# Kernel tuning notes

Hardware: AMD Instinct MI355X
Metric: run time of the kernel (lower is better)

Reference implementation:

```python
import jax, jax.numpy as jnp
import numpy as np

N = 100000
F = 128

def shifted_softplus(x):
    return jax.nn.softplus(x) - jnp.log(2.0).astype(x.dtype)

def setup_inputs() -> dict:
    key = jax.random.key(0)
    ks = jax.random.split(key, 8)
    scale = 1.0 / np.sqrt(F)
    s = jax.random.normal(ks[0], (N, F), dtype=jnp.float32)
    v = jax.random.normal(ks[1], (N, F, 3), dtype=jnp.float32)
    U_w = jax.random.uniform(ks[2], (F, F), dtype=jnp.float32, minval=-scale, maxval=scale)
    V_w = jax.random.uniform(ks[3], (F, F), dtype=jnp.float32, minval=-scale, maxval=scale)
    scale2 = 1.0 / np.sqrt(2 * F)
    a_w1 = jax.random.uniform(ks[4], (F, 2 * F), dtype=jnp.float32, minval=-scale2, maxval=scale2)
    a_b1 = jax.random.uniform(ks[5], (F,), dtype=jnp.float32, minval=-scale2, maxval=scale2)
    a_w2 = jax.random.uniform(ks[6], (3 * F, F), dtype=jnp.float32, minval=-scale, maxval=scale)
    a_b2 = jax.random.uniform(ks[7], (3 * F,), dtype=jnp.float32, minval=-scale, maxval=scale)
    return {"s": s, "v": v, "U_w": U_w, "V_w": V_w,
            "a_w1": a_w1, "a_b1": a_b1, "a_w2": a_w2, "a_b2": a_b2}

def reference(s, v, U_w, V_w, a_w1, a_b1, a_w2, a_b2):
    # Vector linears along feature dim: (N,F,3) x (Fout,Fin) -> (N,F,3)
    Uv = jnp.einsum('nfc,gf->ngc', v, U_w)
    Vv = jnp.einsum('nfc,gf->ngc', v, V_w)
    Vv_norm_sq = jnp.sum(Vv * Vv, axis=-1)          # (N,F)
    mlp_in = jnp.concatenate([s, Vv_norm_sq], axis=-1)  # (N,2F)
    h = shifted_softplus(mlp_in @ a_w1.T + a_b1)     # (N,F)
    a = h @ a_w2.T + a_b2                            # (N,3F)
    a_ss, a_sv, a_vv = jnp.split(a, 3, axis=-1)
    inner = jnp.sum(Uv * Vv, axis=-1)                # (N,F)
    s_new = s + a_ss + a_sv * inner
    v_new = v + a_vv[:, :, None] * Uv
    return (s_new, v_new)
```

## Files before the change

kernel.cpp:

```cpp
#include <hip/hip_runtime.h>

#define F 128
#define TILE 32
#define NTHR 512
#define NBLK 256

typedef __attribute__((ext_vector_type(8))) __bf16 bf16x8;
typedef __attribute__((ext_vector_type(4))) float f32x4;
typedef __attribute__((ext_vector_type(8))) unsigned short us8;
typedef __attribute__((ext_vector_type(4))) unsigned short us4;
typedef __attribute__((ext_vector_type(2))) unsigned short us2;

struct f3 { float x, y, z; };

__device__ __forceinline__ unsigned short f2bf(float x) {
    __bf16 h = (__bf16)x;
    return __builtin_bit_cast(unsigned short, h);
}
__device__ __forceinline__ float bf2f(unsigned short u) {
    unsigned x = ((unsigned)u) << 16;
    return __builtin_bit_cast(float, x);
}
__device__ __forceinline__ bf16x8 pack8(float4 a, float4 b) {
    us8 t;
    t[0] = f2bf(a.x); t[1] = f2bf(a.y); t[2] = f2bf(a.z); t[3] = f2bf(a.w);
    t[4] = f2bf(b.x); t[5] = f2bf(b.y); t[6] = f2bf(b.z); t[7] = f2bf(b.w);
    return __builtin_bit_cast(bf16x8, t);
}

__device__ __forceinline__ void gload16(const float* g, const unsigned short* l) {
    __builtin_amdgcn_global_load_lds(
        (const __attribute__((address_space(1))) void*)g,
        (__attribute__((address_space(3))) void*)l, 16, 0, 0);
}

#define RAWV 0
#define A1B  24576
#define A1S  136
#define A2B  37632
#define A2S  264
#define A3B  46080
#define A3S  136
#define SHSZ 50432

__global__ __launch_bounds__(256)
void prep_w(const float* __restrict__ Uw, const float* __restrict__ Vw,
            const float* __restrict__ aw1, const float* __restrict__ aw2,
            unsigned short* __restrict__ wbf)
{
    int i = (blockIdx.x * 256 + threadIdx.x) * 4;
    const float* src; int off;
    if (i < 16384)      { src = Uw;  off = i; }
    else if (i < 32768) { src = Vw;  off = i - 16384; }
    else if (i < 65536) { src = aw1; off = i - 32768; }
    else                { src = aw2; off = i - 65536; }
    float4 x = *(const float4*)&src[off];
    us4 o;
    o[0] = f2bf(x.x); o[1] = f2bf(x.y); o[2] = f2bf(x.z); o[3] = f2bf(x.w);
    *(us4*)&wbf[i] = o;
}

template<bool PRE>
__global__ __launch_bounds__(NTHR) __attribute__((amdgpu_waves_per_eu(2, 2)))
void painn_main(const float* __restrict__ s, const float* __restrict__ v,
                const float* __restrict__ Uw, const float* __restrict__ Vw,
                const float* __restrict__ aw1, const float* __restrict__ ab1,
                const float* __restrict__ aw2, const float* __restrict__ ab2,
                const unsigned short* __restrict__ wbf,
                float* __restrict__ out, int Ntot)
{
    __shared__ __align__(16) unsigned short SH[SHSZ];

    const int tid  = threadIdx.x;
    const int lane = tid & 63;
    const int w    = tid >> 6;
    const int l15  = lane & 15;
    const int kp   = lane >> 4;
    const int col  = (w << 4) | l15;
    const size_t NF = (size_t)Ntot * F;
    const int NT   = Ntot / TILE;

    const unsigned short* wU  = wbf;
    const unsigned short* wV  = wbf + 16384;
    const unsigned short* wW1 = wbf + 32768;
    const unsigned short* wW2 = wbf + 65536;

    const float b1  = ab1[col];
    const float bss = ab2[col];
    const float bsv = ab2[F + col];
    const float bvv = ab2[2 * F + col];

    const int vf0  = lane << 1;
    const int srow = tid >> 4;
    const int sf0  = (tid & 15) << 3;

    const float* rawv = (const float*)&SH[RAWV];

    float4 sp0, sp1;

    {
        int t0 = blockIdx.x;
        const float* vsrc = v + (size_t)t0 * TILE * 384;
        #pragma unroll
        for (int j = 0; j < 6; ++j) {
            int ofs = (w + j * 8) * 256;
            gload16(vsrc + ofs + lane * 4, &SH[RAWV + ofs * 2]);
        }
        const float* ssrc = s + (size_t)t0 * TILE * 128 + srow * 128 + sf0;
        sp0 = *(const float4*)ssrc;
        sp1 = *(const float4*)(ssrc + 4);
    }
    asm volatile("s_waitcnt vmcnt(0)" ::: "memory");

    for (int t = blockIdx.x; t < NT; t += NBLK) {
        asm volatile("s_waitcnt vmcnt(8)" ::: "memory");
        __builtin_amdgcn_s_barrier();

        bf16x8 bU[4], bV[4], bW1[8], bWs[4], bWt[4], bWv[4];
        if constexpr (PRE) {
            #pragma unroll
            for (int ks = 0; ks < 4; ++ks) {
                int k0 = (ks << 5) + (kp << 3);
                bU[ks]  = *(const bf16x8*)&wU[col * F + k0];
                bV[ks]  = *(const bf16x8*)&wV[col * F + k0];
                bWs[ks] = *(const bf16x8*)&wW2[(0 * F + col) * F + k0];
                bWt[ks] = *(const bf16x8*)&wW2[(1 * F + col) * F + k0];
                bWv[ks] = *(const bf16x8*)&wW2[(2 * F + col) * F + k0];
            }
            #pragma unroll
            for (int ks = 0; ks < 8; ++ks) {
                int k0 = (ks << 5) + (kp << 3);
                bW1[ks] = *(const bf16x8*)&wW1[col * 256 + k0];
            }
        } else {
            #pragma unroll
            for (int ks = 0; ks < 4; ++ks) {
                int k0 = (ks << 5) + (kp << 3);
                const float4* p;
                p = (const float4*)&Uw[col * F + k0];              bU[ks]  = pack8(p[0], p[1]);
                p = (const float4*)&Vw[col * F + k0];              bV[ks]  = pack8(p[0], p[1]);
                p = (const float4*)&aw2[(size_t)(0*F+col)*F + k0]; bWs[ks] = pack8(p[0], p[1]);
                p = (const float4*)&aw2[(size_t)(1*F+col)*F + k0]; bWt[ks] = pack8(p[0], p[1]);
                p = (const float4*)&aw2[(size_t)(2*F+col)*F + k0]; bWv[ks] = pack8(p[0], p[1]);
            }
            #pragma unroll
            for (int ks = 0; ks < 8; ++ks) {
                int k0 = (ks << 5) + (kp << 3);
                const float4* p = (const float4*)&aw1[col * 256 + k0];
                bW1[ks] = pack8(p[0], p[1]);
            }
        }
        __builtin_amdgcn_sched_barrier(0);

        #pragma unroll
        for (int it = 0; it < 4; ++it) {
            int nl = w + (it << 3);
            const float2* src = (const float2*)&rawv[nl * 384 + vf0 * 3];
            float2 ab = src[0], cd = src[1], ef = src[2];
            us2 p;
            p[0] = f2bf(ab.x); p[1] = f2bf(cd.y); *(us2*)&SH[A1B + (0 * TILE + nl) * A1S + vf0] = p;
            p[0] = f2bf(ab.y); p[1] = f2bf(ef.x); *(us2*)&SH[A1B + (1 * TILE + nl) * A1S + vf0] = p;
            p[0] = f2bf(cd.x); p[1] = f2bf(ef.y); *(us2*)&SH[A1B + (2 * TILE + nl) * A1S + vf0] = p;
        }
        {
            us4 t0, t1;
            t0[0] = f2bf(sp0.x); t0[1] = f2bf(sp0.y); t0[2] = f2bf(sp0.z); t0[3] = f2bf(sp0.w);
            t1[0] = f2bf(sp1.x); t1[1] = f2bf(sp1.y); t1[2] = f2bf(sp1.z); t1[3] = f2bf(sp1.w);
            *(us4*)&SH[A2B + srow * A2S + sf0]     = t0;
            *(us4*)&SH[A2B + srow * A2S + sf0 + 4] = t1;
        }
        asm volatile("s_waitcnt lgkmcnt(0)" ::: "memory");
        __builtin_amdgcn_s_barrier();
        __builtin_amdgcn_sched_barrier(0);

        if (t + NBLK < NT) {
            int t2 = t + NBLK;
            const float* vsrc = v + (size_t)t2 * TILE * 384;
            #pragma unroll
            for (int j = 0; j < 6; ++j) {
                int ofs = (w + j * 8) * 256;
                gload16(vsrc + ofs + lane * 4, &SH[RAWV + ofs * 2]);
            }
            const float* ssrc = s + (size_t)t2 * TILE * 128 + srow * 128 + sf0;
            sp0 = *(const float4*)ssrc;
            sp1 = *(const float4*)(ssrc + 4);
        }
        __builtin_amdgcn_sched_barrier(0);

        float inr[2][4], nrm[2][4];
        us4 pU[6];
        #pragma unroll
        for (int nt = 0; nt < 2; ++nt)
            #pragma unroll
            for (int r = 0; r < 4; ++r) { inr[nt][r] = 0.f; nrm[nt][r] = 0.f; }
        #pragma unroll
        for (int c = 0; c < 3; ++c) {
            f32x4 aU[2], aV[2];
            aU[0] = (f32x4){0.f,0.f,0.f,0.f}; aU[1] = (f32x4){0.f,0.f,0.f,0.f};
            aV[0] = (f32x4){0.f,0.f,0.f,0.f}; aV[1] = (f32x4){0.f,0.f,0.f,0.f};
            #pragma unroll
            for (int ks = 0; ks < 4; ++ks) {
                #pragma unroll
                for (int nt = 0; nt < 2; ++nt) {
                    bf16x8 a = *(const bf16x8*)&SH[A1B + ((c * 2 + nt) * 16 + l15) * A1S + (ks << 5) + (kp << 3)];
                    aU[nt] = __builtin_amdgcn_mfma_f32_16x16x32_bf16(a, bU[ks], aU[nt], 0, 0, 0);
                    aV[nt] = __builtin_amdgcn_mfma_f32_16x16x32_bf16(a, bV[ks], aV[nt], 0, 0, 0);
                }
            }
            #pragma unroll
            for (int nt = 0; nt < 2; ++nt) {
                us4 q;
                #pragma unroll
                for (int r = 0; r < 4; ++r) {
                    nrm[nt][r] += aV[nt][r] * aV[nt][r];
                    inr[nt][r] += aU[nt][r] * aV[nt][r];
                    q[r] = f2bf(aU[nt][r]);
                }
                pU[c * 2 + nt] = q;
            }
        }
        #pragma unroll
        for (int nt = 0; nt < 2; ++nt) {
            #pragma unroll
            for (int r = 0; r < 4; ++r) {
                int row = nt * 16 + (kp << 2) + r;
                SH[A2B + row * A2S + 128 + col] = f2bf(nrm[nt][r]);
            }
        }
        asm volatile("s_waitcnt lgkmcnt(0)" ::: "memory");
        __builtin_amdgcn_s_barrier();

        f32x4 accH[2];
        accH[0] = (f32x4){0.f,0.f,0.f,0.f}; accH[1] = (f32x4){0.f,0.f,0.f,0.f};
        #pragma unroll
        for (int ks = 0; ks < 8; ++ks) {
            int k0 = (ks << 5) + (kp << 3);
            #pragma unroll
            for (int nt = 0; nt < 2; ++nt) {
                bf16x8 a = *(const bf16x8*)&SH[A2B + (nt * 16 + l15) * A2S + k0];
                accH[nt] = __builtin_amdgcn_mfma_f32_16x16x32_bf16(a, bW1[ks], accH[nt], 0, 0, 0);
            }
        }
        #pragma unroll
        for (int nt = 0; nt < 2; ++nt) {
            #pragma unroll
            for (int r = 0; r < 4; ++r) {
                float x = accH[nt][r] + b1;
                float hsp = fmaxf(x, 0.f) + __logf(1.f + __expf(-fabsf(x))) - 0.69314718056f;
                int row = nt * 16 + (kp << 2) + r;
                SH[A3B + row * A3S + col] = f2bf(hsp);
            }
        }
        asm volatile("s_waitcnt lgkmcnt(0)" ::: "memory");
        __builtin_amdgcn_s_barrier();

        f32x4 accA[2], accS[2], accT[2];
        #pragma unroll
        for (int i = 0; i < 2; ++i) {
            accA[i] = (f32x4){0.f,0.f,0.f,0.f};
            accS[i] = (f32x4){0.f,0.f,0.f,0.f};
            accT[i] = (f32x4){0.f,0.f,0.f,0.f};
        }
        #pragma unroll
        for (int ks = 0; ks < 4; ++ks) {
            int k0 = (ks << 5) + (kp << 3);
            #pragma unroll
            for (int nt = 0; nt < 2; ++nt) {
                bf16x8 a = *(const bf16x8*)&SH[A3B + (nt * 16 + l15) * A3S + k0];
                accS[nt] = __builtin_amdgcn_mfma_f32_16x16x32_bf16(a, bWs[ks], accS[nt], 0, 0, 0);
                accT[nt] = __builtin_amdgcn_mfma_f32_16x16x32_bf16(a, bWt[ks], accT[nt], 0, 0, 0);
                accA[nt] = __builtin_amdgcn_mfma_f32_16x16x32_bf16(a, bWv[ks], accA[nt], 0, 0, 0);
            }
        }

        #pragma unroll
        for (int nt = 0; nt < 2; ++nt) {
            #pragma unroll
            for (int r = 0; r < 4; ++r) {
                int nl = nt * 16 + (kp << 2) + r;
                int n  = t * TILE + nl;
                float avv = accA[nt][r] + bvv;
                size_t base = ((size_t)n * F + col) * 3;
                f3 val;
                val.x = bf2f(SH[A1B + (0 * TILE + nl) * A1S + col]) + avv * bf2f(pU[0 * 2 + nt][r]);
                val.y = bf2f(SH[A1B + (1 * TILE + nl) * A1S + col]) + avv * bf2f(pU[1 * 2 + nt][r]);
                val.z = bf2f(SH[A1B + (2 * TILE + nl) * A1S + col]) + avv * bf2f(pU[2 * 2 + nt][r]);
                *(f3*)&out[NF + base] = val;
                float sres = bf2f(SH[A2B + nl * A2S + col]);
                out[(size_t)n * F + col] = sres + (accS[nt][r] + bss) + (accT[nt][r] + bsv) * inr[nt][r];
            }
        }
    }
}

extern "C" void kernel_launch(void* const* d_in, const int* in_sizes, int n_in,
                              void* d_out, int out_size, void* d_ws, size_t ws_size,
                              hipStream_t stream) {
    (void)n_in; (void)out_size;
    const float* s   = (const float*)d_in[0];
    const float* v   = (const float*)d_in[1];
    const float* Uw  = (const float*)d_in[2];
    const float* Vw  = (const float*)d_in[3];
    const float* aw1 = (const float*)d_in[4];
    const float* ab1 = (const float*)d_in[5];
    const float* aw2 = (const float*)d_in[6];
    const float* ab2 = (const float*)d_in[7];
    float* out = (float*)d_out;
    int Ntot = in_sizes[0] / F;

    if (ws_size >= 114688u * sizeof(unsigned short)) {
        unsigned short* wbf = (unsigned short*)d_ws;
        hipLaunchKernelGGL(prep_w, dim3(112), dim3(256), 0, stream, Uw, Vw, aw1, aw2, wbf);
        hipLaunchKernelGGL((painn_main<true>), dim3(NBLK), dim3(NTHR), 0, stream,
                           s, v, Uw, Vw, aw1, ab1, aw2, ab2, wbf, out, Ntot);
    } else {
        hipLaunchKernelGGL((painn_main<false>), dim3(NBLK), dim3(NTHR), 0, stream,
                           s, v, Uw, Vw, aw1, ab1, aw2, ab2, (const unsigned short*)nullptr, out, Ntot);
    }
}
```

Before: 187.2 us.

## Split fused persistent kernel into three per-tile kernels with bf16 workspace intermediates

Replaces the single persistent fused kernel with three non-persistent kernels: one computes Vv norms and the U·V inner product, one runs the MLP and writes s_new, and one recomputes Uv and writes v_new. Each launches one block per tile and uses far less shared memory, allowing higher occupancy in place of the software-pipelined persistent loop. The cost is reading v twice, recomputing U·v, and round-tripping three N×F bf16 intermediates through global memory, plus extra launches and a larger workspace requirement. The fused kernel is kept as a fallback when the workspace is too small.

```diff
diff --git a/kernel.cpp b/kernel.cpp
--- a/kernel.cpp
+++ b/kernel.cpp
@@ -3,21 +3,23 @@
 #define F 128
 #define TILE 32
 #define NTHR 512
-#define NBLK 256
 
 typedef __attribute__((ext_vector_type(8))) __bf16 bf16x8;
 typedef __attribute__((ext_vector_type(4))) float f32x4;
 typedef __attribute__((ext_vector_type(8))) unsigned short us8;
 typedef __attribute__((ext_vector_type(4))) unsigned short us4;
 typedef __attribute__((ext_vector_type(2))) unsigned short us2;
+typedef unsigned short us;
 
 struct f3 { float x, y, z; };
 
-__device__ __forceinline__ unsigned short f2bf(float x) {
+#define MFMA(a,b,c) __builtin_amdgcn_mfma_f32_16x16x32_bf16((a),(b),(c),0,0,0)
+
+__device__ __forceinline__ us f2bf(float x) {
     __bf16 h = (__bf16)x;
-    return __builtin_bit_cast(unsigned short, h);
-}
-__device__ __forceinline__ float bf2f(unsigned short u) {
+    return __builtin_bit_cast(us, h);
+}
+__device__ __forceinline__ float bf2f(us u) {
     unsigned x = ((unsigned)u) << 16;
     return __builtin_bit_cast(float, x);
 }
@@ -27,26 +29,20 @@
     t[4] = f2bf(b.x); t[5] = f2bf(b.y); t[6] = f2bf(b.z); t[7] = f2bf(b.w);
     return __builtin_bit_cast(bf16x8, t);
 }
-
-__device__ __forceinline__ void gload16(const float* g, const unsigned short* l) {
+__device__ __forceinline__ void gload16(const float* g, const us* l) {
     __builtin_amdgcn_global_load_lds(
         (const __attribute__((address_space(1))) void*)g,
         (__attribute__((address_space(3))) void*)l, 16, 0, 0);
 }
-
-#define RAWV 0
-#define A1B  24576
-#define A1S  136
-#define A2B  37632
-#define A2S  264
-#define A3B  46080
-#define A3S  136
-#define SHSZ 50432
+__device__ __forceinline__ void bar_lgkm() {
+    asm volatile("s_waitcnt lgkmcnt(0)" ::: "memory");
+    __builtin_amdgcn_s_barrier();
+}
 
 __global__ __launch_bounds__(256)
 void prep_w(const float* __restrict__ Uw, const float* __restrict__ Vw,
             const float* __restrict__ aw1, const float* __restrict__ aw2,
-            unsigned short* __restrict__ wbf)
+            us* __restrict__ wbf)
 {
     int i = (blockIdx.x * 256 + threadIdx.x) * 4;
     const float* src; int off;
@@ -60,151 +56,377 @@
     *(us4*)&wbf[i] = o;
 }
 
+#define K_RAWV 0
+#define K_VRB  24576
+#define K_OUT  24576
+#define K_SHSZ 36864
+
+__device__ __forceinline__ int k_vr(int crow, int k) {
+    return K_VRB + (((crow << 7) + k) ^ ((crow & 7) << 3));
+}
+
+#define STAGE_AND_CONVERT(vptr, t)                                              \
+    {                                                                           \
+        const float* vsrc = (vptr) + (size_t)(t) * (TILE * 384);                \
+        _Pragma("unroll")                                                       \
+        for (int j = 0; j < 6; ++j) {                                           \
+            int ofs = (w + j * 8) * 256;                                        \
+            gload16(vsrc + ofs + lane * 4, &SH[K_RAWV + ofs * 2]);              \
+        }                                                                       \
+    }                                                                           \
+    asm volatile("s_waitcnt vmcnt(0)" ::: "memory");                            \
+    __builtin_amdgcn_s_barrier();                                               \
+    {                                                                           \
+        const float* rawv = (const float*)&SH[K_RAWV];                          \
+        _Pragma("unroll")                                                       \
+        for (int it = 0; it < 4; ++it) {                                        \
+            int idx = tid + it * 512, nl = idx >> 6, f0 = (idx & 63) << 1;      \
+            const float2* src = (const float2*)&rawv[nl * 384 + f0 * 3];        \
+            float2 ab = src[0], cd = src[1], ef = src[2];                       \
+            us2 p;                                                              \
+            p[0]=f2bf(ab.x); p[1]=f2bf(cd.y); *(us2*)&SH[k_vr(0*TILE+nl,f0)]=p; \
+            p[0]=f2bf(ab.y); p[1]=f2bf(ef.x); *(us2*)&SH[k_vr(1*TILE+nl,f0)]=p; \
+            p[0]=f2bf(cd.x); p[1]=f2bf(ef.y); *(us2*)&SH[k_vr(2*TILE+nl,f0)]=p; \
+        }                                                                       \
+    }                                                                           \
+    bar_lgkm();
+
+__global__ __launch_bounds__(NTHR, 4)
+void k1_uv(const float* __restrict__ v, const us* __restrict__ wbf,
+           us* __restrict__ wnrm, us* __restrict__ winr, int Ntot)
+{
+    __shared__ __align__(16) us SH[K_SHSZ];
+    const int tid = threadIdx.x, lane = tid & 63, w = tid >> 6;
+    const int l15 = lane & 15, kp = lane >> 4;
+    const int col = (w << 4) | l15;
+    const int t   = blockIdx.x;
+
+    STAGE_AND_CONVERT(v, t)
+
+    bf16x8 bU[4], bV[4];
+    #pragma unroll
+    for (int ks = 0; ks < 4; ++ks) {
+        int k0 = (ks << 5) + (kp << 3);
+        bU[ks] = *(const bf16x8*)&wbf[col * F + k0];
+        bV[ks] = *(const bf16x8*)&wbf[16384 + col * F + k0];
+    }
+    float nrm[2][4], inr[2][4];
+    #pragma unroll
+    for (int c = 0; c < 3; ++c) {
+        f32x4 aU[2], aV[2];
+        aU[0]=(f32x4){0,0,0,0}; aU[1]=(f32x4){0,0,0,0};
+        aV[0]=(f32x4){0,0,0,0}; aV[1]=(f32x4){0,0,0,0};
+        #pragma unroll
+        for (int ks = 0; ks < 4; ++ks) {
+            #pragma unroll
+            for (int nt = 0; nt < 2; ++nt) {
+                bf16x8 a = *(const bf16x8*)&SH[k_vr(c*TILE + nt*16 + l15, (ks<<5)+(kp<<3))];
+                aU[nt] = MFMA(a, bU[ks], aU[nt]);
+                aV[nt] = MFMA(a, bV[ks], aV[nt]);
+            }
+        }
+        #pragma unroll
+        for (int nt = 0; nt < 2; ++nt)
+            #pragma unroll
+            for (int r = 0; r < 4; ++r) {
+                float uu = aU[nt][r], vv = aV[nt][r];
+                if (c == 0) { nrm[nt][r] = vv*vv; inr[nt][r] = uu*vv; }
+                else        { nrm[nt][r] += vv*vv; inr[nt][r] += uu*vv; }
+            }
+    }
+    bar_lgkm();
+    #pragma unroll
+    for (int nt = 0; nt < 2; ++nt)
+        #pragma unroll
+        for (int r = 0; r < 4; ++r) {
+            int row = nt * 16 + (kp << 2) + r;
+            SH[K_OUT + row * 128 + col]        = f2bf(nrm[nt][r]);
+            SH[K_OUT + 4096 + row * 128 + col] = f2bf(inr[nt][r]);
+        }
+    bar_lgkm();
+    *(us8*)&wnrm[(size_t)t * 4096 + tid * 8] = *(const us8*)&SH[K_OUT + tid * 8];
+    *(us8*)&winr[(size_t)t * 4096 + tid * 8] = *(const us8*)&SH[K_OUT + 4096 + tid * 8];
+}
+
+#define M_A2S 264
+#define M_A3B 8448
+#define M_A3S 136
+#define M_SHSZ 12800
+
+__global__ __launch_bounds__(NTHR, 4)
+void k2_mlp(const float* __restrict__ s, const us* __restrict__ wbf,
+            const float* __restrict__ ab1, const float* __restrict__ ab2,
+            const us* __restrict__ wnrm, const us* __restrict__ winr,
+            us* __restrict__ wavv, float* __restrict__ out, int Ntot)
+{
+    __shared__ __align__(16) us SH[M_SHSZ];
+    const int tid = threadIdx.x, lane = tid & 63, w = tid >> 6;
+    const int l15 = lane & 15, kp = lane >> 4;
+    const int col = (w << 4) | l15;
+    const int t   = blockIdx.x;
+    const int srow = tid >> 4, sf0 = (tid & 15) << 3;
+
+    {
+        const float4* sp = (const float4*)&s[(size_t)t * TILE * 128 + srow * 128 + sf0];
+        float4 x = sp[0], y = sp[1];
+        us4 t0, t1;
+        t0[0]=f2bf(x.x); t0[1]=f2bf(x.y); t0[2]=f2bf(x.z); t0[3]=f2bf(x.w);
+        t1[0]=f2bf(y.x); t1[1]=f2bf(y.y); t1[2]=f2bf(y.z); t1[3]=f2bf(y.w);
+        *(us4*)&SH[srow * M_A2S + sf0]     = t0;
+        *(us4*)&SH[srow * M_A2S + sf0 + 4] = t1;
+        us8 nv = *(const us8*)&wnrm[(size_t)t * 4096 + tid * 8];
+        *(us8*)&SH[srow * M_A2S + 128 + sf0] = nv;
+    }
+    bar_lgkm();
+
+    f32x4 accH[2];
+    accH[0]=(f32x4){0,0,0,0}; accH[1]=(f32x4){0,0,0,0};
+    #pragma unroll
+    for (int ks = 0; ks < 8; ++ks) {
+        int k0 = (ks << 5) + (kp << 3);
+        bf16x8 bw = *(const bf16x8*)&wbf[32768 + col * 256 + k0];
+        #pragma unroll
+        for (int nt = 0; nt < 2; ++nt) {
+            bf16x8 a = *(const bf16x8*)&SH[(nt * 16 + l15) * M_A2S + k0];
+            accH[nt] = MFMA(a, bw, accH[nt]);
+        }
+    }
+    float b1 = ab1[col];
+    #pragma unroll
+    for (int nt = 0; nt < 2; ++nt)
+        #pragma unroll
+        for (int r = 0; r < 4; ++r) {
+            float x = accH[nt][r] + b1;
+            float hsp = fmaxf(x, 0.f) + __logf(1.f + __expf(-fabsf(x))) - 0.69314718056f;
+            int row = nt * 16 + (kp << 2) + r;
+            SH[M_A3B + row * M_A3S + col] = f2bf(hsp);
+        }
+    bar_lgkm();
+
+    f32x4 accS[2], accT[2], accA[2];
+    #pragma unroll
+    for (int i = 0; i < 2; ++i) {
+        accS[i]=(f32x4){0,0,0,0}; accT[i]=(f32x4){0,0,0,0}; accA[i]=(f32x4){0,0,0,0};
+    }
+    #pragma unroll
+    for (int ks = 0; ks < 4; ++ks) {
+        int k0 = (ks << 5) + (kp << 3);
+        bf16x8 bws = *(const bf16x8*)&wbf[65536 + (0 * F + col) * F + k0];
+        bf16x8 bwt = *(const bf16x8*)&wbf[65536 + (1 * F + col) * F + k0];
+        bf16x8 bwv = *(const bf16x8*)&wbf[65536 + (2 * F + col) * F + k0];
+        #pragma unroll
+        for (int nt = 0; nt < 2; ++nt) {
+            bf16x8 a = *(const bf16x8*)&SH[M_A3B + (nt * 16 + l15) * M_A3S + k0];
+            accS[nt] = MFMA(a, bws, accS[nt]);
+            accT[nt] = MFMA(a, bwt, accT[nt]);
+            accA[nt] = MFMA(a, bwv, accA[nt]);
+        }
+    }
+
+    float bss = ab2[col], bsv = ab2[F + col], bvv = ab2[2 * F + col];
+    #pragma unroll
+    for (int nt = 0; nt < 2; ++nt)
+        #pragma unroll
+        for (int r = 0; r < 4; ++r) {
+            int nl = nt * 16 + (kp << 2) + r;
+            size_t n = (size_t)t * TILE + nl;
+            float inner = bf2f(winr[n * 128 + col]);
+            float sres  = bf2f(SH[nl * M_A2S + col]);
+            out[n * 128 + col] = sres + (accS[nt][r] + bss) + (accT[nt][r] + bsv) * inner;
+        }
+    bar_lgkm();
+    #pragma unroll
+    for (int nt = 0; nt < 2; ++nt)
+        #pragma unroll
+        for (int r = 0; r < 4; ++r) {
+            int row = nt * 16 + (kp << 2) + r;
+            SH[row * 128 + col] = f2bf(accA[nt][r] + bvv);
+        }
+    bar_lgkm();
+    *(us8*)&wavv[(size_t)t * 4096 + tid * 8] = *(const us8*)&SH[tid * 8];
+}
+
+__global__ __launch_bounds__(NTHR, 4)
+void k3_vnew(const float* __restrict__ v, const us* __restrict__ wbf,
+             const us* __restrict__ wavv, float* __restrict__ out, int Ntot)
+{
+    __shared__ __align__(16) us SH[K_SHSZ];
+    const int tid = threadIdx.x, lane = tid & 63, w = tid >> 6;
+    const int l15 = lane & 15, kp = lane >> 4;
+    const int col = (w << 4) | l15;
+    const int t   = blockIdx.x;
+    const size_t NF = (size_t)Ntot * F;
+
+    STAGE_AND_CONVERT(v, t)
+
+    bf16x8 bU[4];
+    #pragma unroll
+    for (int ks = 0; ks < 4; ++ks) {
+        int k0 = (ks << 5) + (kp << 3);
+        bU[ks] = *(const bf16x8*)&wbf[col * F + k0];
+    }
+    us4 pU[3][2];
+    #pragma unroll
+    for (int c = 0; c < 3; ++c) {
+        f32x4 aU[2];
+        aU[0]=(f32x4){0,0,0,0}; aU[1]=(f32x4){0,0,0,0};
+        #pragma unroll
+        for (int ks = 0; ks < 4; ++ks) {
+            #pragma unroll
+            for (int nt = 0; nt < 2; ++nt) {
+                bf16x8 a = *(const bf16x8*)&SH[k_vr(c*TILE + nt*16 + l15, (ks<<5)+(kp<<3))];
+                aU[nt] = MFMA(a, bU[ks], aU[nt]);
+            }
+        }
+        #pragma unroll
+        for (int nt = 0; nt < 2; ++nt) {
+            us4 q;
+            #pragma unroll
+            for (int r = 0; r < 4; ++r) q[r] = f2bf(aU[nt][r]);
+            pU[c][nt] = q;
+        }
+    }
+
+    const float* rawv = (const float*)&SH[K_RAWV];
+    #pragma unroll
+    for (int nt = 0; nt < 2; ++nt)
+        #pragma unroll
+        for (int r = 0; r < 4; ++r) {
+            int nl = nt * 16 + (kp << 2) + r;
+            size_t n = (size_t)t * TILE + nl;
+            float avv = bf2f(wavv[n * 128 + col]);
+            f3 val;
+            val.x = rawv[nl * 384 + col * 3 + 0] + avv * bf2f(pU[0][nt][r]);
+            val.y = rawv[nl * 384 + col * 3 + 1] + avv * bf2f(pU[1][nt][r]);
+            val.z = rawv[nl * 384 + col * 3 + 2] + avv * bf2f(pU[2][nt][r]);
+            *(f3*)&out[NF + (n * 128 + col) * 3] = val;
+        }
+}
+
+#define FD_RAWV 0
+#define FD_A1B  24576
+#define FD_A1S  136
+#define FD_A2B  37632
+#define FD_A2S  264
+#define FD_A3B  46080
+#define FD_A3S  136
+#define FD_SHSZ 50432
+#define FD_NBLK 256
+
 template<bool PRE>
 __global__ __launch_bounds__(NTHR) __attribute__((amdgpu_waves_per_eu(2, 2)))
-void painn_main(const float* __restrict__ s, const float* __restrict__ v,
-                const float* __restrict__ Uw, const float* __restrict__ Vw,
-                const float* __restrict__ aw1, const float* __restrict__ ab1,
-                const float* __restrict__ aw2, const float* __restrict__ ab2,
-                const unsigned short* __restrict__ wbf,
-                float* __restrict__ out, int Ntot)
+void fused_fb(const float* __restrict__ s, const float* __restrict__ v,
+              const float* __restrict__ Uw, const float* __restrict__ Vw,
+              const float* __restrict__ aw1, const float* __restrict__ ab1,
+              const float* __restrict__ aw2, const float* __restrict__ ab2,
+              const us* __restrict__ wbf, float* __restrict__ out, int Ntot)
 {
-    __shared__ __align__(16) unsigned short SH[SHSZ];
-
-    const int tid  = threadIdx.x;
-    const int lane = tid & 63;
-    const int w    = tid >> 6;
-    const int l15  = lane & 15;
-    const int kp   = lane >> 4;
-    const int col  = (w << 4) | l15;
+    __shared__ __align__(16) us SH[FD_SHSZ];
+    const int tid = threadIdx.x, lane = tid & 63, w = tid >> 6;
+    const int l15 = lane & 15, kp = lane >> 4;
+    const int col = (w << 4) | l15;
     const size_t NF = (size_t)Ntot * F;
-    const int NT   = Ntot / TILE;
-
-    const unsigned short* wU  = wbf;
-    const unsigned short* wV  = wbf + 16384;
-    const unsigned short* wW1 = wbf + 32768;
-    const unsigned short* wW2 = wbf + 65536;
-
-    const float b1  = ab1[col];
-    const float bss = ab2[col];
-    const float bsv = ab2[F + col];
-    const float bvv = ab2[2 * F + col];
-
-    const int vf0  = lane << 1;
-    const int srow = tid >> 4;
-    const int sf0  = (tid & 15) << 3;
-
-    const float* rawv = (const float*)&SH[RAWV];
-
+    const int NT = Ntot / TILE;
+    const us* wU  = wbf;
+    const us* wV  = wbf + 16384;
+    const us* wW1 = wbf + 32768;
+    const us* wW2 = wbf + 65536;
+    const float b1 = ab1[col], bss = ab2[col], bsv = ab2[F+col], bvv = ab2[2*F+col];
+    const int srow = tid >> 4, sf0 = (tid & 15) << 3;
+    const float* rawv = (const float*)&SH[FD_RAWV];
     float4 sp0, sp1;
-
     {
         int t0 = blockIdx.x;
         const float* vsrc = v + (size_t)t0 * TILE * 384;
         #pragma unroll
         for (int j = 0; j < 6; ++j) {
             int ofs = (w + j * 8) * 256;
-            gload16(vsrc + ofs + lane * 4, &SH[RAWV + ofs * 2]);
+            gload16(vsrc + ofs + lane * 4, &SH[FD_RAWV + ofs * 2]);
         }
         const float* ssrc = s + (size_t)t0 * TILE * 128 + srow * 128 + sf0;
-        sp0 = *(const float4*)ssrc;
-        sp1 = *(const float4*)(ssrc + 4);
+        sp0 = *(const float4*)ssrc; sp1 = *(const float4*)(ssrc + 4);
     }
     asm volatile("s_waitcnt vmcnt(0)" ::: "memory");
-
-    for (int t = blockIdx.x; t < NT; t += NBLK) {
+    for (int t = blockIdx.x; t < NT; t += FD_NBLK) {
         asm volatile("s_waitcnt vmcnt(8)" ::: "memory");
         __builtin_amdgcn_s_barrier();
-
         bf16x8 bU[4], bV[4], bW1[8], bWs[4], bWt[4], bWv[4];
         if constexpr (PRE) {
             #pragma unroll
             for (int ks = 0; ks < 4; ++ks) {
                 int k0 = (ks << 5) + (kp << 3);
-                bU[ks]  = *(const bf16x8*)&wU[col * F + k0];
-                bV[ks]  = *(const bf16x8*)&wV[col * F + k0];
-                bWs[ks] = *(const bf16x8*)&wW2[(0 * F + col) * F + k0];
-                bWt[ks] = *(const bf16x8*)&wW2[(1 * F + col) * F + k0];
-                bWv[ks] = *(const bf16x8*)&wW2[(2 * F + col) * F + k0];
-            }
-            #pragma unroll
-            for (int ks = 0; ks < 8; ++ks) {
-                int k0 = (ks << 5) + (kp << 3);
-                bW1[ks] = *(const bf16x8*)&wW1[col * 256 + k0];
-            }
+                bU[ks] = *(const bf16x8*)&wU[col*F+k0];
+                bV[ks] = *(const bf16x8*)&wV[col*F+k0];
+                bWs[ks] = *(const bf16x8*)&wW2[(0*F+col)*F+k0];
+                bWt[ks] = *(const bf16x8*)&wW2[(1*F+col)*F+k0];
+                bWv[ks] = *(const bf16x8*)&wW2[(2*F+col)*F+k0];
+            }
+            #pragma unroll
+            for (int ks = 0; ks < 8; ++ks)
+                bW1[ks] = *(const bf16x8*)&wW1[col*256 + (ks<<5)+(kp<<3)];
         } else {
             #pragma unroll
             for (int ks = 0; ks < 4; ++ks) {
                 int k0 = (ks << 5) + (kp << 3);
                 const float4* p;
-                p = (const float4*)&Uw[col * F + k0];              bU[ks]  = pack8(p[0], p[1]);
-                p = (const float4*)&Vw[col * F + k0];              bV[ks]  = pack8(p[0], p[1]);
-                p = (const float4*)&aw2[(size_t)(0*F+col)*F + k0]; bWs[ks] = pack8(p[0], p[1]);
-                p = (const float4*)&aw2[(size_t)(1*F+col)*F + k0]; bWt[ks] = pack8(p[0], p[1]);
-                p = (const float4*)&aw2[(size_t)(2*F+col)*F + k0]; bWv[ks] = pack8(p[0], p[1]);
+                p = (const float4*)&Uw[col*F+k0];               bU[ks]=pack8(p[0],p[1]);
+                p = (const float4*)&Vw[col*F+k0];               bV[ks]=pack8(p[0],p[1]);
+                p = (const float4*)&aw2[(size_t)(0*F+col)*F+k0]; bWs[ks]=pack8(p[0],p[1]);
+                p = (const float4*)&aw2[(size_t)(1*F+col)*F+k0]; bWt[ks]=pack8(p[0],p[1]);
+                p = (const float4*)&aw2[(size_t)(2*F+col)*F+k0]; bWv[ks]=pack8(p[0],p[1]);
             }
             #pragma unroll
             for (int ks = 0; ks < 8; ++ks) {
-                int k0 = (ks << 5) + (kp << 3);
-                const float4* p = (const float4*)&aw1[col * 256 + k0];
+                const float4* p = (const float4*)&aw1[col*256 + (ks<<5)+(kp<<3)];
                 bW1[ks] = pack8(p[0], p[1]);
             }
         }
         __builtin_amdgcn_sched_barrier(0);
-
         #pragma unroll
         for (int it = 0; it < 4; ++it) {
             int nl = w + (it << 3);
-            const float2* src = (const float2*)&rawv[nl * 384 + vf0 * 3];
+            const float2* src = (const float2*)&rawv[nl * 384 + (lane << 1) * 3];
             float2 ab = src[0], cd = src[1], ef = src[2];
+            int vf0 = lane << 1;
             us2 p;
-            p[0] = f2bf(ab.x); p[1] = f2bf(cd.y); *(us2*)&SH[A1B + (0 * TILE + nl) * A1S + vf0] = p;
-            p[0] = f2bf(ab.y); p[1] = f2bf(ef.x); *(us2*)&SH[A1B + (1 * TILE + nl) * A1S + vf0] = p;
-            p[0] = f2bf(cd.x); p[1] = f2bf(ef.y); *(us2*)&SH[A1B + (2 * TILE + nl) * A1S + vf0] = p;
+            p[0]=f2bf(ab.x); p[1]=f2bf(cd.y); *(us2*)&SH[FD_A1B+(0*TILE+nl)*FD_A1S+vf0]=p;
+            p[0]=f2bf(ab.y); p[1]=f2bf(ef.x); *(us2*)&SH[FD_A1B+(1*TILE+nl)*FD_A1S+vf0]=p;
+            p[0]=f2bf(cd.x); p[1]=f2bf(ef.y); *(us2*)&SH[FD_A1B+(2*TILE+nl)*FD_A1S+vf0]=p;
         }
         {
             us4 t0, t1;
-            t0[0] = f2bf(sp0.x); t0[1] = f2bf(sp0.y); t0[2] = f2bf(sp0.z); t0[3] = f2bf(sp0.w);
-            t1[0] = f2bf(sp1.x); t1[1] = f2bf(sp1.y); t1[2] = f2bf(sp1.z); t1[3] = f2bf(sp1.w);
-            *(us4*)&SH[A2B + srow * A2S + sf0]     = t0;
-            *(us4*)&SH[A2B + srow * A2S + sf0 + 4] = t1;
-        }
-        asm volatile("s_waitcnt lgkmcnt(0)" ::: "memory");
-        __builtin_amdgcn_s_barrier();
-        __builtin_amdgcn_sched_barrier(0);
-
-        if (t + NBLK < NT) {
-            int t2 = t + NBLK;
+            t0[0]=f2bf(sp0.x); t0[1]=f2bf(sp0.y); t0[2]=f2bf(sp0.z); t0[3]=f2bf(sp0.w);
+            t1[0]=f2bf(sp1.x); t1[1]=f2bf(sp1.y); t1[2]=f2bf(sp1.z); t1[3]=f2bf(sp1.w);
+            *(us4*)&SH[FD_A2B + srow*FD_A2S + sf0]     = t0;
+            *(us4*)&SH[FD_A2B + srow*FD_A2S + sf0 + 4] = t1;
+        }
+        bar_lgkm();
+        if (t + FD_NBLK < NT) {
+            int t2 = t + FD_NBLK;
             const float* vsrc = v + (size_t)t2 * TILE * 384;
             #pragma unroll
             for (int j = 0; j < 6; ++j) {
                 int ofs = (w + j * 8) * 256;
-                gload16(vsrc + ofs + lane * 4, &SH[RAWV + ofs * 2]);
+                gload16(vsrc + ofs + lane * 4, &SH[FD_RAWV + ofs * 2]);
             }
             const float* ssrc = s + (size_t)t2 * TILE * 128 + srow * 128 + sf0;
-            sp0 = *(const float4*)ssrc;
-            sp1 = *(const float4*)(ssrc + 4);
+            sp0 = *(const float4*)ssrc; sp1 = *(const float4*)(ssrc + 4);
         }
         __builtin_amdgcn_sched_barrier(0);
-
         float inr[2][4], nrm[2][4];
         us4 pU[6];
         #pragma unroll
-        for (int nt = 0; nt < 2; ++nt)
-            #pragma unroll
-            for (int r = 0; r < 4; ++r) { inr[nt][r] = 0.f; nrm[nt][r] = 0.f; }
-        #pragma unroll
         for (int c = 0; c < 3; ++c) {
             f32x4 aU[2], aV[2];
-            aU[0] = (f32x4){0.f,0.f,0.f,0.f}; aU[1] = (f32x4){0.f,0.f,0.f,0.f};
-            aV[0] = (f32x4){0.f,0.f,0.f,0.f}; aV[1] = (f32x4){0.f,0.f,0.f,0.f};
+            aU[0]=(f32x4){0,0,0,0}; aU[1]=(f32x4){0,0,0,0};
+            aV[0]=(f32x4){0,0,0,0}; aV[1]=(f32x4){0,0,0,0};
             #pragma unroll
             for (int ks = 0; ks < 4; ++ks) {
                 #pragma unroll
                 for (int nt = 0; nt < 2; ++nt) {
-                    bf16x8 a = *(const bf16x8*)&SH[A1B + ((c * 2 + nt) * 16 + l15) * A1S + (ks << 5) + (kp << 3)];
-                    aU[nt] = __builtin_amdgcn_mfma_f32_16x16x32_bf16(a, bU[ks], aU[nt], 0, 0, 0);
-                    aV[nt] = __builtin_amdgcn_mfma_f32_16x16x32_bf16(a, bV[ks], aV[nt], 0, 0, 0);
+                    bf16x8 a = *(const bf16x8*)&SH[FD_A1B + ((c*2+nt)*16 + l15)*FD_A1S + (ks<<5)+(kp<<3)];
+                    aU[nt] = MFMA(a, bU[ks], aU[nt]);
+                    aV[nt] = MFMA(a, bV[ks], aV[nt]);
                 }
             }
             #pragma unroll
@@ -212,84 +434,72 @@
                 us4 q;
                 #pragma unroll
                 for (int r = 0; r < 4; ++r) {
-                    nrm[nt][r] += aV[nt][r] * aV[nt][r];
-                    inr[nt][r] += aU[nt][r] * aV[nt][r];
-                    q[r] = f2bf(aU[nt][r]);
+                    float uu = aU[nt][r], vv = aV[nt][r];
+                    if (c == 0) { nrm[nt][r]=vv*vv; inr[nt][r]=uu*vv; }
+                    else        { nrm[nt][r]+=vv*vv; inr[nt][r]+=uu*vv; }
+                    q[r] = f2bf(uu);
                 }
-                pU[c * 2 + nt] = q;
-            }
-        }
-        #pragma unroll
-        for (int nt = 0; nt < 2; ++nt) {
-            #pragma unroll
-            for (int r = 0; r < 4; ++r) {
-                int row = nt * 16 + (kp << 2) + r;
-                SH[A2B + row * A2S + 128 + col] = f2bf(nrm[nt][r]);
-            }
-        }
-        asm volatile("s_waitcnt lgkmcnt(0)" ::: "memory");
-        __builtin_amdgcn_s_barrier();
-
+                pU[c*2+nt] = q;
+            }
+        }
+        #pragma unroll
+        for (int nt = 0; nt < 2; ++nt)
+            #pragma unroll
+            for (int r = 0; r < 4; ++r)
+                SH[FD_A2B + (nt*16+(kp<<2)+r)*FD_A2S + 128 + col] = f2bf(nrm[nt][r]);
+        bar_lgkm();
         f32x4 accH[2];
-        accH[0] = (f32x4){0.f,0.f,0.f,0.f}; accH[1] = (f32x4){0.f,0.f,0.f,0.f};
+        accH[0]=(f32x4){0,0,0,0}; accH[1]=(f32x4){0,0,0,0};
         #pragma unroll
         for (int ks = 0; ks < 8; ++ks) {
             int k0 = (ks << 5) + (kp << 3);
             #pragma unroll
             for (int nt = 0; nt < 2; ++nt) {
-                bf16x8 a = *(const bf16x8*)&SH[A2B + (nt * 16 + l15) * A2S + k0];
-                accH[nt] = __builtin_amdgcn_mfma_f32_16x16x32_bf16(a, bW1[ks], accH[nt], 0, 0, 0);
-            }
-        }
-        #pragma unroll
-        for (int nt = 0; nt < 2; ++nt) {
+                bf16x8 a = *(const bf16x8*)&SH[FD_A2B + (nt*16+l15)*FD_A2S + k0];
+                accH[nt] = MFMA(a, bW1[ks], accH[nt]);
+            }
+        }
+        #pragma unroll
+        for (int nt = 0; nt < 2; ++nt)
             #pragma unroll
             for (int r = 0; r < 4; ++r) {
                 float x = accH[nt][r] + b1;
                 float hsp = fmaxf(x, 0.f) + __logf(1.f + __expf(-fabsf(x))) - 0.69314718056f;
-                int row = nt * 16 + (kp << 2) + r;
-                SH[A3B + row * A3S + col] = f2bf(hsp);
-            }
-        }
-        asm volatile("s_waitcnt lgkmcnt(0)" ::: "memory");
-        __builtin_amdgcn_s_barrier();
-
-        f32x4 accA[2], accS[2], accT[2];
+                SH[FD_A3B + (nt*16+(kp<<2)+r)*FD_A3S + col] = f2bf(hsp);
+            }
+        bar_lgkm();
+        f32x4 accS[2], accT[2], accA[2];
         #pragma unroll
         for (int i = 0; i < 2; ++i) {
-            accA[i] = (f32x4){0.f,0.f,0.f,0.f};
-            accS[i] = (f32x4){0.f,0.f,0.f,0.f};
-            accT[i] = (f32x4){0.f,0.f,0.f,0.f};
+            accS[i]=(f32x4){0,0,0,0}; accT[i]=(f32x4){0,0,0,0}; accA[i]=(f32x4){0,0,0,0};
         }
         #pragma unroll
         for (int ks = 0; ks < 4; ++ks) {
             int k0 = (ks << 5) + (kp << 3);
             #pragma unroll
             for (int nt = 0; nt < 2; ++nt) {
-                bf16x8 a = *(const bf16x8*)&SH[A3B + (nt * 16 + l15) * A3S + k0];
-                accS[nt] = __builtin_amdgcn_mfma_f32_16x16x32_bf16(a, bWs[ks], accS[nt], 0, 0, 0);
-                accT[nt] = __builtin_amdgcn_mfma_f32_16x16x32_bf16(a, bWt[ks], accT[nt], 0, 0, 0);
-                accA[nt] = __builtin_amdgcn_mfma_f32_16x16x32_bf16(a, bWv[ks], accA[nt], 0, 0, 0);
-            }
-        }
-
-        #pragma unroll
-        for (int nt = 0; nt < 2; ++nt) {
+                bf16x8 a = *(const bf16x8*)&SH[FD_A3B + (nt*16+l15)*FD_A3S + k0];
+                accS[nt] = MFMA(a, bWs[ks], accS[nt]);
+                accT[nt] = MFMA(a, bWt[ks], accT[nt]);
+                accA[nt] = MFMA(a, bWv[ks], accA[nt]);
+            }
+        }
+        #pragma unroll
+        for (int nt = 0; nt < 2; ++nt)
             #pragma unroll
             for (int r = 0; r < 4; ++r) {
-                int nl = nt * 16 + (kp << 2) + r;
+                int nl = nt*16 + (kp<<2) + r;
                 int n  = t * TILE + nl;
                 float avv = accA[nt][r] + bvv;
                 size_t base = ((size_t)n * F + col) * 3;
                 f3 val;
-                val.x = bf2f(SH[A1B + (0 * TILE + nl) * A1S + col]) + avv * bf2f(pU[0 * 2 + nt][r]);
-                val.y = bf2f(SH[A1B + (1 * TILE + nl) * A1S + col]) + avv * bf2f(pU[1 * 2 + nt][r]);
-                val.z = bf2f(SH[A1B + (2 * TILE + nl) * A1S + col]) + avv * bf2f(pU[2 * 2 + nt][r]);
+                val.x = bf2f(SH[FD_A1B+(0*TILE+nl)*FD_A1S+col]) + avv*bf2f(pU[0*2+nt][r]);
+                val.y = bf2f(SH[FD_A1B+(1*TILE+nl)*FD_A1S+col]) + avv*bf2f(pU[1*2+nt][r]);
+                val.z = bf2f(SH[FD_A1B+(2*TILE+nl)*FD_A1S+col]) + avv*bf2f(pU[2*2+nt][r]);
                 *(f3*)&out[NF + base] = val;
-                float sres = bf2f(SH[A2B + nl * A2S + col]);
-                out[(size_t)n * F + col] = sres + (accS[nt][r] + bss) + (accT[nt][r] + bsv) * inr[nt][r];
-            }
-        }
+                float sres = bf2f(SH[FD_A2B + nl*FD_A2S + col]);
+                out[(size_t)n*F + col] = sres + (accS[nt][r]+bss) + (accT[nt][r]+bsv)*inr[nt][r];
+            }
     }
 }
 
@@ -307,14 +517,27 @@
     const float* ab2 = (const float*)d_in[7];
     float* out = (float*)d_out;
     int Ntot = in_sizes[0] / F;
-
-    if (ws_size >= 114688u * sizeof(unsigned short)) {
-        unsigned short* wbf = (unsigned short*)d_ws;
+    int NTb  = Ntot / TILE;
+
+    const size_t WSZ_W = 114688ull * 2;
+    const size_t PER   = (size_t)Ntot * F * 2;
+
+    if (ws_size >= WSZ_W + 3 * PER) {
+        us* wbf  = (us*)d_ws;
+        us* wnrm = (us*)((char*)d_ws + WSZ_W);
+        us* winr = wnrm + (size_t)Ntot * F;
+        us* wavv = winr + (size_t)Ntot * F;
         hipLaunchKernelGGL(prep_w, dim3(112), dim3(256), 0, stream, Uw, Vw, aw1, aw2, wbf);
-        hipLaunchKernelGGL((painn_main<true>), dim3(NBLK), dim3(NTHR), 0, stream,
+        hipLaunchKernelGGL(k1_uv,   dim3(NTb), dim3(NTHR), 0, stream, v, wbf, wnrm, winr, Ntot);
+        hipLaunchKernelGGL(k2_mlp,  dim3(NTb), dim3(NTHR), 0, stream, s, wbf, ab1, ab2, wnrm, winr, wavv, out, Ntot);
+        hipLaunchKernelGGL(k3_vnew, dim3(NTb), dim3(NTHR), 0, stream, v, wbf, wavv, out, Ntot);
+    } else if (ws_size >= WSZ_W) {
+        us* wbf = (us*)d_ws;
+        hipLaunchKernelGGL(prep_w, dim3(112), dim3(256), 0, stream, Uw, Vw, aw1, aw2, wbf);
+        hipLaunchKernelGGL((fused_fb<true>), dim3(FD_NBLK), dim3(NTHR), 0, stream,
                            s, v, Uw, Vw, aw1, ab1, aw2, ab2, wbf, out, Ntot);
     } else {
-        hipLaunchKernelGGL((painn_main<false>), dim3(NBLK), dim3(NTHR), 0, stream,
-                           s, v, Uw, Vw, aw1, ab1, aw2, ab2, (const unsigned short*)nullptr, out, Ntot);
-    }
-}
+        hipLaunchKernelGGL((fused_fb<false>), dim3(FD_NBLK), dim3(NTHR), 0, stream,
+                           s, v, Uw, Vw, aw1, ab1, aw2, ab2, (const us*)nullptr, out, Ntot);
+    }
+}
```

Result: slower. 206.3 us (+10.2%).
